# Performance work log

Hardware: AMD Instinct MI355X
Metric: run time of the kernel (lower is better)

Reference implementation:

```python
import jax, jax.numpy as jnp
import numpy as np

S = 3072       # packed sequence length
DIM = 1280     # hidden dim
H = 16         # num heads
HD = DIM // H  # head dim = 80
NEG = -1e9     # additive mask value for cross-segment entries


def setup_inputs() -> dict:
    key = jax.random.key(0)
    ks = jax.random.split(key, 6)
    x = jax.random.normal(ks[0], (S, DIM), jnp.float32)
    # rope angle table [S, HD//2]
    rotary_pos_emb = jax.random.uniform(ks[1], (S, HD // 2), jnp.float32, 0.0, 2.0 * np.pi)
    # 4 equal image segments packed together
    cu_seqlens = jnp.array([0, 768, 1536, 2304, 3072], jnp.int32)
    w_qkv = jax.random.normal(ks[2], (3 * DIM, DIM), jnp.float32) * 0.02
    b_qkv = jax.random.normal(ks[3], (3 * DIM,), jnp.float32) * 0.02
    w_proj = jax.random.normal(ks[4], (DIM, DIM), jnp.float32) * 0.02
    b_proj = jax.random.normal(ks[5], (DIM,), jnp.float32) * 0.02
    return {"x": x, "cu_seqlens": cu_seqlens, "rotary_pos_emb": rotary_pos_emb,
            "w_qkv": w_qkv, "b_qkv": b_qkv, "w_proj": w_proj, "b_proj": b_proj}


def _rope(t, cos, sin):
    # t: [S, H, HD]; cos/sin: [S, 1, HD]
    t1, t2 = jnp.split(t, 2, axis=-1)
    rot = jnp.concatenate([-t2, t1], axis=-1)
    return t * cos + rot * sin


def reference(x, cu_seqlens, rotary_pos_emb, w_qkv, b_qkv, w_proj, b_proj):
    s, d = x.shape
    qkv = (x @ w_qkv.T + b_qkv).reshape(s, 3, H, HD)
    q, k, v = qkv[:, 0], qkv[:, 1], qkv[:, 2]  # each [S, H, HD]

    # NeoX-style rope with tiled (repeated) freqs, computed in fp32
    cos = jnp.cos(rotary_pos_emb)
    sin = jnp.sin(rotary_pos_emb)
    cos = jnp.concatenate([cos, cos], axis=-1)[:, None, :]  # [S,1,HD]
    sin = jnp.concatenate([sin, sin], axis=-1)[:, None, :]
    q = _rope(q.astype(jnp.float32), cos, sin).astype(x.dtype)
    k = _rope(k.astype(jnp.float32), cos, sin).astype(x.dtype)

    # block-diagonal varlen mask from cu_seqlens: segment id per position
    seg = jnp.searchsorted(cu_seqlens, jnp.arange(s), side='right') - 1  # [S]
    mask = jnp.where(seg[:, None] == seg[None, :], 0.0, NEG).astype(x.dtype)  # [S,S]

    scale = 1.0 / np.sqrt(HD).astype(np.float32)
    scores = jnp.einsum('qhd,khd->hqk', q, k) * scale + mask[None]  # [H,S,S]
    attn = jax.nn.softmax(scores, axis=-1)
    out = jnp.einsum('hqk,khd->qhd', attn, v).reshape(s, d)  # [S, DIM]
    return out @ w_proj.T + b_proj
```

## Files before the change

### kernel.cpp

```cpp
#include <hip/hip_runtime.h>


typedef __bf16 bf16;
typedef __bf16 bf16x4 __attribute__((ext_vector_type(4)));
typedef __bf16 bf16x8 __attribute__((ext_vector_type(8)));
typedef float f32x4 __attribute__((ext_vector_type(4)));
typedef float f32x16 __attribute__((ext_vector_type(16)));
typedef unsigned int u32;

constexpr int S = 3072;
constexpr int DIM = 1280;
constexpr int H = 16;
constexpr int HD = 80;
constexpr int KDP = 128;
constexpr int NQKV = 3 * DIM;

constexpr int BM = 192;
constexpr int MB_A = S / BM;
constexpr int NB_B = NQKV / 256;
constexpr int NKT = DIM / 32;
constexpr int ASL = BM * 32 * 2;
constexpr int SLOT = ASL + 16384;

constexpr float QSCALE = 1.4426950408889634f / 8.94427190999916f;

__device__ __forceinline__ void gload_lds16(const void* g, void* l) {
  __builtin_amdgcn_global_load_lds(
      (const __attribute__((address_space(1))) void*)g,
      (__attribute__((address_space(3))) void*)l, 16, 0, 0);
}

__device__ __forceinline__ u32 pkbf2(float a, float b) {
  union { bf16 h[2]; u32 w; } u;
  u.h[0] = (bf16)a; u.h[1] = (bf16)b;
  return u.w;
}

__device__ __forceinline__ int swv(int s) {
  return ((((s >> 3) & 31) ^ ((s & 7) << 2)) << 2);
}

constexpr long PA_CHUNKS = (long)MB_A * NKT * (ASL / 16);
constexpr long PB_CHUNKS = (long)NB_B * NKT * 1024;
constexpr long PW_CHUNKS = (long)DIM * DIM / 8;
constexpr long KP_CHUNKS = (long)H * S * 48 / 8;
constexpr long CS_CHUNKS = (long)S * 40 / 8;
constexpr long TOT_CHUNKS = PA_CHUNKS + PB_CHUNKS + PW_CHUNKS + KP_CHUNKS + CS_CHUNKS;

__global__ __launch_bounds__(256) void pack_inputs(
    const float* __restrict__ x, const float* __restrict__ wq,
    const float* __restrict__ wp, const float* __restrict__ rope,
    bf16* __restrict__ pA, bf16* __restrict__ pB, bf16* __restrict__ wp16,
    bf16* __restrict__ Kb, float* __restrict__ ctab, float* __restrict__ stab) {
  long t = (long)blockIdx.x * 256 + threadIdx.x;
  if (t < PA_CHUNKS) {
    const int blk = (int)(t / (NKT * 768)), rem = (int)(t % (NKT * 768));
    const int kt = rem / 768, c = rem - kt * 768;
    const int lin = c * 16;
    const int logi = lin ^ (((lin >> 7) & 7) << 4);
    const int row = logi >> 6, col = (logi & 63) >> 1;
    const float* src = x + (size_t)(blk * BM + row) * DIM + kt * 32 + col;
    float4 v0 = *(const float4*)src;
    float4 v1 = *(const float4*)(src + 4);
    bf16x8 o = {(bf16)v0.x, (bf16)v0.y, (bf16)v0.z, (bf16)v0.w,
                (bf16)v1.x, (bf16)v1.y, (bf16)v1.z, (bf16)v1.w};
    *(bf16x8*)(pA + t * 8) = o;
  } else if (t < PA_CHUNKS + PB_CHUNKS) {
    long t2 = t - PA_CHUNKS;
    const int blk = (int)(t2 / (NKT * 1024)), rem = (int)(t2 % (NKT * 1024));
    const int kt = rem >> 10, c = rem & 1023;
    const int lin = c * 16;
    const int logi = lin ^ (((lin >> 7) & 7) << 4);
    const int row = logi >> 6, col = (logi & 63) >> 1;
    int grow = blk * 256 + row;
    if (grow < 2560) {
      const int ty = grow / 1280, rm = grow % 1280;
      const int h = rm / 80, p = rm % 80;
      grow = ty * 1280 + h * 80 + (p >> 1) + (p & 1) * 40;
    }
    const float* src = wq + (size_t)grow * DIM + kt * 32 + col;
    float4 v0 = *(const float4*)src;
    float4 v1 = *(const float4*)(src + 4);
    bf16x8 o = {(bf16)v0.x, (bf16)v0.y, (bf16)v0.z, (bf16)v0.w,
                (bf16)v1.x, (bf16)v1.y, (bf16)v1.z, (bf16)v1.w};
    *(bf16x8*)(pB + t2 * 8) = o;
  } else if (t < PA_CHUNKS + PB_CHUNKS + PW_CHUNKS) {
    long t2 = t - PA_CHUNKS - PB_CHUNKS;
    const float* src = wp + t2 * 8;
    float4 v0 = *(const float4*)src;
    float4 v1 = *(const float4*)(src + 4);
    bf16x8 o = {(bf16)v0.x, (bf16)v0.y, (bf16)v0.z, (bf16)v0.w,
                (bf16)v1.x, (bf16)v1.y, (bf16)v1.z, (bf16)v1.w};
    *(bf16x8*)(wp16 + t2 * 8) = o;
  } else if (t < PA_CHUNKS + PB_CHUNKS + PW_CHUNKS + KP_CHUNKS) {
    long t2 = t - PA_CHUNKS - PB_CHUNKS - PW_CHUNKS;
    const int h = (int)(t2 / (S * 6)), r = (int)(t2 % (S * 6));
    const int s = r / 6, cc = r % 6;
    bf16x8 z = {};
    *(bf16x8*)(Kb + ((size_t)h * S + s) * KDP + 80 + cc * 8) = z;
  } else {
    long t3 = t - PA_CHUNKS - PB_CHUNKS - PW_CHUNKS - KP_CHUNKS;
#pragma unroll
    for (int k = 0; k < 8; k++) {
      const int idx = (int)(t3 * 8 + k);
      const int s = idx / 40, a = idx % 40;
      float sn, cs;
      __sincosf(rope[idx], &sn, &cs);
      ctab[a * S + s] = cs;
      stab[a * S + s] = sn;
    }
  }
}

__global__ __launch_bounds__(512, 2) void gemm256(
    const bf16* __restrict__ pA, const bf16* __restrict__ pB,
    const float* __restrict__ bias, const float* __restrict__ ctab,
    const float* __restrict__ stab, bf16* __restrict__ Qb,
    bf16* __restrict__ Kb, bf16* __restrict__ VTb) {
  extern __shared__ char lds[];
  const int tid = threadIdx.x;
  const int w = tid >> 6, lane = tid & 63;
  const int r15 = lane & 15, b4 = lane >> 4;
  const int wr = w >> 2, wc = w & 3;
  const int nwg = gridDim.x * gridDim.y;
  const int orig = blockIdx.y * gridDim.x + blockIdx.x;
  const int xcd = orig % 8, loc = orig / 8;
  const int qq = nwg / 8, rq = nwg % 8;
  const int swzid =
      (xcd < rq ? xcd * (qq + 1) : rq * (qq + 1) + (xcd - rq) * qq) + loc;
  const int nb = swzid % gridDim.x, mb = swzid / gridDim.x;
  const int m0 = mb * BM;
  const char* aPanel = (const char*)pA + (size_t)mb * NKT * ASL;
  const char* bPanel = (const char*)pB + (size_t)nb * NKT * 16384;
  auto stageA = [&](int kt) {
    char* s = lds + (kt & 3) * SLOT;
    const char* g = aPanel + (size_t)kt * ASL;
    gload_lds16(g + tid * 16, s + tid * 16);
    if (tid < 256)
      gload_lds16(g + 8192 + tid * 16, s + 8192 + tid * 16);
  };
  auto stageB = [&](int kt) {
    char* s = lds + (kt & 3) * SLOT + ASL;
    const char* g = bPanel + (size_t)kt * 16384;
    gload_lds16(g + tid * 16, s + tid * 16);
    gload_lds16(g + 8192 + tid * 16, s + 8192 + tid * 16);
  };
  f32x4 acc[6][4] = {};
  stageA(0); stageB(0); stageA(1); stageB(1); stageA(2); stageB(2);
  if (tid < 256) asm volatile("s_waitcnt vmcnt(8)" ::: "memory");
  else           asm volatile("s_waitcnt vmcnt(6)" ::: "memory");
  __builtin_amdgcn_s_barrier();
  for (int kt = 0; kt < NKT; ++kt) {
    const char* As = lds + (kt & 3) * SLOT;
    const char* Bs = As + ASL;
    const bool pf = (kt + 3 < NKT);
    bf16x8 afr[3], bfr[4];
#pragma unroll
    for (int i = 0; i < 3; i++) {
      int a = (wr * 96 + i * 16 + r15) * 64 + b4 * 16;
      a ^= ((a >> 7) & 7) << 4;
      afr[i] = *(const bf16x8*)(As + a);
    }
#pragma unroll
    for (int j = 0; j < 4; j++) {
      int a = (wc * 64 + j * 16 + r15) * 64 + b4 * 16;
      a ^= ((a >> 7) & 7) << 4;
      bfr[j] = *(const bf16x8*)(Bs + a);
    }
    if (pf) stageA(kt + 3);
    asm volatile("" ::: "memory");
    __builtin_amdgcn_s_barrier();
    __builtin_amdgcn_s_setprio(1);
#pragma unroll
    for (int i = 0; i < 3; i++)
#pragma unroll
      for (int j = 0; j < 4; j++)
        acc[i][j] = __builtin_amdgcn_mfma_f32_16x16x32_bf16(afr[i], bfr[j],
                                                            acc[i][j], 0, 0, 0);
    __builtin_amdgcn_s_setprio(0);
    asm volatile("" ::: "memory");
    __builtin_amdgcn_s_barrier();
#pragma unroll
    for (int i = 0; i < 3; i++) {
      int a = (wr * 96 + 48 + i * 16 + r15) * 64 + b4 * 16;
      a ^= ((a >> 7) & 7) << 4;
      afr[i] = *(const bf16x8*)(As + a);
    }
    if (pf) stageB(kt + 3);
    asm volatile("" ::: "memory");
    __builtin_amdgcn_s_barrier();
    __builtin_amdgcn_s_setprio(1);
#pragma unroll
    for (int i = 0; i < 3; i++)
#pragma unroll
      for (int j = 0; j < 4; j++)
        acc[3 + i][j] = __builtin_amdgcn_mfma_f32_16x16x32_bf16(
            afr[i], bfr[j], acc[3 + i][j], 0, 0, 0);
    __builtin_amdgcn_s_setprio(0);
    const int rem = NKT - 2 - kt;
    if (tid < 256) {
      if (rem >= 2)      asm volatile("s_waitcnt vmcnt(8)" ::: "memory");
      else if (rem == 1) asm volatile("s_waitcnt vmcnt(4)" ::: "memory");
      else if (rem == 0) asm volatile("s_waitcnt vmcnt(0)" ::: "memory");
      else               asm volatile("" ::: "memory");
    } else {
      if (rem >= 2)      asm volatile("s_waitcnt vmcnt(6)" ::: "memory");
      else if (rem == 1) asm volatile("s_waitcnt vmcnt(3)" ::: "memory");
      else if (rem == 0) asm volatile("s_waitcnt vmcnt(0)" ::: "memory");
      else               asm volatile("" ::: "memory");
    }
    __builtin_amdgcn_s_barrier();
  }
  const int n0 = nb * 256;
  const int type = n0 / 1280;
  const int cpart0 = n0 - type * 1280;
  if (type < 2) {
#pragma unroll
    for (int j = 0; j < 4; j++) {
      const int c = wc * 64 + j * 16 + r15;
      const int cp = cpart0 + c;
      const int h = cp / 80, p = cp % 80;
      const int d = (p >> 1) + (p & 1) * 40;
      const float bv = bias[type * 1280 + h * 80 + d];
      const int a = p >> 1;
#pragma unroll
      for (int i = 0; i < 6; i++) {
        const int sl = wr * 96 + i * 16 + b4 * 4;
        f32x4 cs4 = *(const f32x4*)&ctab[a * S + m0 + sl];
        f32x4 sn4 = *(const f32x4*)&stab[a * S + m0 + sl];
#pragma unroll
        for (int r = 0; r < 4; r++) {
          float v = acc[i][j][r] + bv;
          float ov = __shfl_xor(v, 1);
          float res = (p & 1) ? (v * cs4[r] + ov * sn4[r])
                              : (v * cs4[r] - ov * sn4[r]);
          if (type == 0) res *= QSCALE;
          *(bf16*)(lds + (sl + r) * 512 + ((2 * c) ^ (((sl + r) & 7) << 4))) =
              (bf16)res;
        }
      }
    }
    __syncthreads();
#pragma unroll
    for (int t = 0; t < 12; t++) {
      const int task = t * 512 + tid;
      const int sl = task >> 5, c = (task & 31) * 8;
      bf16x8 v = *(const bf16x8*)(lds + sl * 512 + ((2 * c) ^ ((sl & 7) << 4)));
      const int cp = cpart0 + c, h = cp / 80, p = cp % 80;
      bf16* dst = type ? Kb + ((size_t)h * S + m0 + sl) * KDP + p
                       : Qb + ((size_t)h * S + m0 + sl) * HD + p;
      *(bf16x8*)dst = v;
    }
  } else {
#pragma unroll
    for (int j = 0; j < 4; j++) {
      const int c = wc * 64 + j * 16 + r15;
      const float bv = bias[2560 + cpart0 + c];
#pragma unroll
      for (int i = 0; i < 6; i++) {
        const int sl = wr * 96 + i * 16 + b4 * 4;
#pragma unroll
        for (int r = 0; r < 4; r++) {
          *(bf16*)(lds + (sl + r) * 512 + ((2 * c) ^ swv(sl + r))) =
              (bf16)(acc[i][j][r] + bv);
        }
      }
    }
    __syncthreads();
#pragma unroll
    for (int t = 0; t < 12; t++) {
      const int task = t * 512 + tid;
      const int c = task & 255, s0 = (task >> 8) * 8;
      union { bf16 h[8]; bf16x8 v; } o;
#pragma unroll
      for (int e = 0; e < 8; e++)
        o.h[e] = *(const bf16*)(lds + (s0 + e) * 512 + ((2 * c) ^ swv(s0 + e)));
      const int cp = cpart0 + c, h = cp / 80, d = cp % 80;
      *(bf16x8*)(VTb + ((size_t)(h * 80 + d)) * S + m0 + s0) = o.v;
    }
  }
}

__global__ __launch_bounds__(256) void gemm_proj(
    const bf16* __restrict__ A, const bf16* __restrict__ B,
    const float* __restrict__ bias, float* __restrict__ Cout, int M, int N,
    int K) {
  __shared__ bf16 Al[2][64 * 32];
  __shared__ bf16 Bl[2][128 * 32];
  const int tid = threadIdx.x;
  const int w = tid >> 6, lane = tid & 63;
  const int r15 = lane & 15, b4 = lane >> 4;
  const int nwg = gridDim.x * gridDim.y;
  const int orig = blockIdx.y * gridDim.x + blockIdx.x;
  const int swzid = (orig & 7) * (nwg >> 3) + (orig >> 3);
  const int bx = swzid % gridDim.x, by = swzid / gridDim.x;
  const int m0 = by * 64, n0 = bx * 128;
  const int wm = (w >> 1) * 32, wn = (w & 1) * 64;
  f32x4 acc[2][4] = {};
  const int row0 = tid >> 2, ko0 = (tid & 3) * 8;
  const bf16* Ar = A + (size_t)(m0 + row0) * K + ko0;
  const bf16* Br0 = B + (size_t)(n0 + row0) * K + ko0;
  const bf16* Br1 = B + (size_t)(n0 + row0 + 64) * K + ko0;

  auto stage = [&](int buf, int k0) {
    gload_lds16(Ar + k0, (char*)Al[buf] + tid * 16);
    gload_lds16(Br0 + k0, (char*)Bl[buf] + tid * 16);
    gload_lds16(Br1 + k0, (char*)Bl[buf] + 4096 + tid * 16);
  };

  stage(0, 0);
  int cur = 0;
  for (int k0 = 0; k0 < K; k0 += 32) {
    __syncthreads();
    if (k0 + 32 < K) stage(cur ^ 1, k0 + 32);
    bf16x8 af[2], bfr[4];
#pragma unroll
    for (int i = 0; i < 2; i++)
      af[i] = *(const bf16x8*)((const char*)Al[cur] + (wm + i * 16 + r15) * 64 + b4 * 16);
#pragma unroll
    for (int j = 0; j < 4; j++)
      bfr[j] = *(const bf16x8*)((const char*)Bl[cur] + (wn + j * 16 + r15) * 64 + b4 * 16);
#pragma unroll
    for (int i = 0; i < 2; i++)
#pragma unroll
      for (int j = 0; j < 4; j++)
        acc[i][j] = __builtin_amdgcn_mfma_f32_16x16x32_bf16(af[i], bfr[j], acc[i][j], 0, 0, 0);
    cur ^= 1;
  }
#pragma unroll
  for (int j = 0; j < 4; j++) {
    const int n = n0 + wn + j * 16 + r15;
    const float bv = bias[n];
#pragma unroll
    for (int i = 0; i < 2; i++) {
      const int mr = m0 + wm + i * 16 + b4 * 4;
#pragma unroll
      for (int r = 0; r < 4; r++)
        Cout[(size_t)(mr + r) * N + n] = acc[i][j][r] + bv;
    }
  }
}

__global__ __launch_bounds__(256, 3) void attn_kern(
    const bf16* __restrict__ Qg, const bf16* __restrict__ Kg,
    const bf16* __restrict__ Vg, const int* __restrict__ cu, int nseg,
    bf16* __restrict__ Out) {
  __shared__ bf16 Kl[2][64 * 128];
  __shared__ bf16 Vl[2][80 * 64];
  const int tid = threadIdx.x, w = tid >> 6, lane = tid & 63;
  const int r31 = lane & 31, hi = lane >> 5;
  const int pair = w >> 1, qs = w & 1;
  const int pt = tid & 127;
  const int nwg = gridDim.x;
  const int orig = blockIdx.x;
  const int swzb = (orig & 7) * (nwg >> 3) + (orig >> 3);
  const int h = swzb / 48, qb = swzb % 48;
  const int q = qb * 64 + qs * 32 + r31;
  int sq = 0, eq = S, lo = 0, hik = S;
  {
    const int qlo = qb * 64, qhi = qb * 64 + 63;
#pragma unroll
    for (int i = 0; i < 8; i++) {
      if (i >= nseg) break;
      int a = cu[i], b = cu[i + 1];
      if (q >= a && q < b) { sq = a; eq = b; }
      if (qlo >= a && qlo < b) lo = a;
      if (qhi >= a && qhi < b) hik = b;
    }
  }
  bf16x8 qf[5];
  {
    const bf16* qrow = Qg + ((size_t)h * S + q) * HD + hi * 8;
#pragma unroll
    for (int kk = 0; kk < 5; kk++) qf[kk] = *(const bf16x8*)(qrow + kk * 16);
  }
  int kdst[8], ksrc[8], vdst[5], vsrc[5];
#pragma unroll
  for (int c = 0; c < 8; c++) {
    int lin = (c * 128 + pt) * 16;
    int row = lin >> 8, colb = (lin & 255) ^ ((row & 15) << 4);
    kdst[c] = lin; ksrc[c] = row * KDP + colb / 2;
  }
#pragma unroll
  for (int c = 0; c < 5; c++) {
    int lin = (c * 128 + pt) * 16;
    int row = lin >> 7, colb = (lin & 127) ^ ((row & 7) << 4);
    vdst[c] = lin; vsrc[c] = row * S + colb / 2;
  }
  const bf16* Kbase = Kg + (size_t)h * S * KDP;
  const bf16* Vbase = Vg + (size_t)h * HD * S;
  char* Klp = (char*)Kl[pair];
  char* Vlp = (char*)Vl[pair];
  auto stage = [&](int k0) {
#pragma unroll
    for (int c = 0; c < 8; c++)
      gload_lds16(Kbase + (size_t)k0 * KDP + ksrc[c], Klp + kdst[c]);
#pragma unroll
    for (int c = 0; c < 5; c++)
      gload_lds16(Vbase + vsrc[c] + k0, Vlp + vdst[c]);
  };
  f32x16 o0 = {}, o1 = {}, o2 = {};
  float m = -1e30f, l = 0.f;
  const int nt = (hik - lo) >> 6;
  const int nit = (nt + 1) >> 1;
  for (int i = 0; i < nit; ++i) {
    const int t = 2 * i + pair;
    const bool act = t < nt;
    const int k0 = lo + t * 64;
    __syncthreads();
    if (act) stage(k0);
    asm volatile("s_waitcnt vmcnt(0)" ::: "memory");
    __syncthreads();
    if (!act) continue;
    f32x16 st0 = {}, st1 = {};
    __builtin_amdgcn_s_setprio(1);
#pragma unroll
    for (int kk = 0; kk < 5; kk++) {
      const int colb = kk * 32 + hi * 16;
      bf16x8 kf0 = *(const bf16x8*)(Klp + r31 * 256 + (colb ^ ((r31 & 15) << 4)));
      bf16x8 kf1 = *(const bf16x8*)(Klp + (32 + r31) * 256 + (colb ^ ((r31 & 15) << 4)));
      st0 = __builtin_amdgcn_mfma_f32_32x32x16_bf16(kf0, qf[kk], st0, 0, 0, 0);
      st1 = __builtin_amdgcn_mfma_f32_32x32x16_bf16(kf1, qf[kk], st1, 0, 0, 0);
    }
    __builtin_amdgcn_s_setprio(0);
    float tm = -3e38f;
    if (k0 >= sq && k0 + 63 < eq) {
#pragma unroll
      for (int j = 0; j < 16; j++) {
        tm = fmaxf(tm, st0[j]);
        tm = fmaxf(tm, st1[j]);
      }
    } else {
#pragma unroll
      for (int j = 0; j < 16; j++) {
        const int crow = (j & 3) + 8 * (j >> 2) + 4 * hi;
        int key0 = k0 + crow, key1 = k0 + 32 + crow;
        st0[j] = (key0 >= sq && key0 < eq) ? st0[j] : -1e30f;
        st1[j] = (key1 >= sq && key1 < eq) ? st1[j] : -1e30f;
        tm = fmaxf(tm, st0[j]);
        tm = fmaxf(tm, st1[j]);
      }
    }
    tm = fmaxf(tm, __shfl_xor(tm, 32));
    if (!__all(tm <= m + 8.f)) {
      const float mn = fmaxf(m, tm);
      const float alpha = __builtin_amdgcn_exp2f(m - mn);
      o0 *= alpha; o1 *= alpha; o2 *= alpha;
      l *= alpha;
      m = mn;
    }
    float rs = 0.f;
    u32 wd0[4][2], wd1[4][2];
#pragma unroll
    for (int g2 = 0; g2 < 4; g2++) {
#pragma unroll
      for (int hh = 0; hh < 2; hh++) {
        float a0 = __builtin_amdgcn_exp2f(st0[g2 * 4 + 2 * hh] - m);
        float a1 = __builtin_amdgcn_exp2f(st0[g2 * 4 + 2 * hh + 1] - m);
        float b0 = __builtin_amdgcn_exp2f(st1[g2 * 4 + 2 * hh] - m);
        float b1 = __builtin_amdgcn_exp2f(st1[g2 * 4 + 2 * hh + 1] - m);
        rs += a0 + a1 + b0 + b1;
        wd0[g2][hh] = pkbf2(a0, a1);
        wd1[g2][hh] = pkbf2(b0, b1);
      }
    }
    rs += __shfl_xor(rs, 32);
    l += rs;
    __builtin_amdgcn_s_setprio(1);
#pragma unroll
    for (int kk = 0; kk < 4; kk++) {
      const int g2o = (kk & 1) * 2 + hi;
      const int g2s = (kk & 1) * 2 + (hi ^ 1);
      u32 own0, own1, snd0, snd1;
      if (kk < 2) {
        own0 = wd0[g2o][0]; own1 = wd0[g2o][1];
        snd0 = wd0[g2s][0]; snd1 = wd0[g2s][1];
      } else {
        own0 = wd1[g2o][0]; own1 = wd1[g2o][1];
        snd0 = wd1[g2s][0]; snd1 = wd1[g2s][1];
      }
      u32 rc0 = (u32)__shfl_xor((int)snd0, 32);
      u32 rc1 = (u32)__shfl_xor((int)snd1, 32);
      union { u32 w[4]; bf16x8 v; } pf;
      if (hi == 0) { pf.w[0] = own0; pf.w[1] = own1; pf.w[2] = rc0; pf.w[3] = rc1; }
      else         { pf.w[0] = rc0;  pf.w[1] = rc1;  pf.w[2] = own0; pf.w[3] = own1; }
      const int colb = kk * 32 + hi * 16;
#pragma unroll
      for (int mt = 0; mt < 3; mt++) {
        int row = mt * 32 + r31;
        row = row < HD ? row : 0;
        bf16x8 vf = *(const bf16x8*)(Vlp + row * 128 + (colb ^ ((row & 7) << 4)));
        f32x16* op = mt == 0 ? &o0 : (mt == 1 ? &o1 : &o2);
        *op = __builtin_amdgcn_mfma_f32_32x32x16_bf16(vf, pf.v, *op, 0, 0, 0);
      }
    }
    __builtin_amdgcn_s_setprio(0);
  }
  __syncthreads();
  float* mb = (float*)Kl;
  if (pair == 1) {
    float* d = mb + ((size_t)qs * 64 + lane) * 50;
    d[0] = m; d[1] = l;
#pragma unroll
    for (int j = 0; j < 16; j++) { d[2 + j] = o0[j]; d[18 + j] = o1[j]; d[34 + j] = o2[j]; }
  }
  __syncthreads();
  if (pair == 0) {
    const float* d = mb + ((size_t)qs * 64 + lane) * 50;
    const float pm = d[0], pl = d[1];
    const float mn = fmaxf(m, pm);
    const float a = __builtin_amdgcn_exp2f(m - mn);
    const float b = __builtin_amdgcn_exp2f(pm - mn);
    const float lt = l * a + pl * b;
    const float inv = 1.f / lt;
    bf16* orow = Out + (size_t)q * DIM + h * HD;
#pragma unroll
    for (int rg = 0; rg < 4; rg++) {
      bf16x4 v0, v1;
#pragma unroll
      for (int e = 0; e < 4; e++) {
        v0[e] = (bf16)((o0[rg * 4 + e] * a + d[2 + rg * 4 + e] * b) * inv);
        v1[e] = (bf16)((o1[rg * 4 + e] * a + d[18 + rg * 4 + e] * b) * inv);
      }
      *(bf16x4*)(orow + 8 * rg + 4 * hi) = v0;
      *(bf16x4*)(orow + 32 + 8 * rg + 4 * hi) = v1;
    }
#pragma unroll
    for (int rg = 0; rg < 2; rg++) {
      bf16x4 v2;
#pragma unroll
      for (int e = 0; e < 4; e++)
        v2[e] = (bf16)((o2[rg * 4 + e] * a + d[34 + rg * 4 + e] * b) * inv);
      *(bf16x4*)(orow + 64 + 8 * rg + 4 * hi) = v2;
    }
  }
}

extern "C" void kernel_launch(void* const* d_in, const int* in_sizes, int n_in,
                              void* d_out, int out_size, void* d_ws,
                              size_t ws_size, hipStream_t stream) {
  const float* x = (const float*)d_in[0];
  const int* cu = (const int*)d_in[1];
  const float* rope = (const float*)d_in[2];
  const float* w_qkv = (const float*)d_in[3];
  const float* b_qkv = (const float*)d_in[4];
  const float* w_proj = (const float*)d_in[5];
  const float* b_proj = (const float*)d_in[6];
  const int nseg = in_sizes[1] - 1;

  bf16* pA = (bf16*)d_ws;
  bf16* pB = pA + (size_t)S * DIM;
  bf16* wp16 = pB + (size_t)NQKV * DIM;
  bf16* Qb = wp16 + (size_t)DIM * DIM;
  bf16* Kb = Qb + (size_t)H * S * HD;
  bf16* VTb = Kb + (size_t)H * S * KDP;
  float* ctab = (float*)(VTb + (size_t)H * HD * S);
  float* stab = ctab + (size_t)S * 40;
  bf16* attn16 = pA;

  pack_inputs<<<(int)(TOT_CHUNKS / 256), 256, 0, stream>>>(
      x, w_qkv, w_proj, rope, pA, pB, wp16, Kb, ctab, stab);
  gemm256<<<dim3(NB_B, MB_A), 512, 114688, stream>>>(
      pA, pB, b_qkv, ctab, stab, Qb, Kb, VTb);
  attn_kern<<<H * 48, 256, 0, stream>>>(Qb, Kb, VTb, cu, nseg, attn16);
  gemm_proj<<<dim3(DIM / 128, S / 64), 256, 0, stream>>>(
      attn16, wp16, b_proj, (float*)d_out, S, DIM, DIM);
}
```

Before: 111.4 us.

## Split attention keys across waves with pre-tiled K/V and no block syncs

New measurement: 118.2 us. 6.2% more time.

```diff
diff --git a/kernel.cpp b/kernel.cpp
--- a/kernel.cpp
+++ b/kernel.cpp
@@ -12,8 +12,8 @@
 constexpr int DIM = 1280;
 constexpr int H = 16;
 constexpr int HD = 80;
-constexpr int KDP = 128;
 constexpr int NQKV = 3 * DIM;
+constexpr int NT32 = S / 32;
 
 constexpr int BM = 192;
 constexpr int MB_A = S / BM;
@@ -21,6 +21,9 @@
 constexpr int NKT = DIM / 32;
 constexpr int ASL = BM * 32 * 2;
 constexpr int SLOT = ASL + 16384;
+
+constexpr int KIMG = 32 * 256;
+constexpr int VIMG = 40 * 128;
 
 constexpr float QSCALE = 1.4426950408889634f / 8.94427190999916f;
 
@@ -94,10 +97,13 @@
     *(bf16x8*)(wp16 + t2 * 8) = o;
   } else if (t < PA_CHUNKS + PB_CHUNKS + PW_CHUNKS + KP_CHUNKS) {
     long t2 = t - PA_CHUNKS - PB_CHUNKS - PW_CHUNKS;
-    const int h = (int)(t2 / (S * 6)), r = (int)(t2 % (S * 6));
-    const int s = r / 6, cc = r % 6;
+    const int h = (int)(t2 / (S * 6)), r0 = (int)(t2 % (S * 6));
+    const int s = r0 / 6, cc = r0 % 6;
+    const int tile = s >> 5, r = s & 31;
+    const int p = 80 + cc * 8;
     bf16x8 z = {};
-    *(bf16x8*)(Kb + ((size_t)h * S + s) * KDP + 80 + cc * 8) = z;
+    *(bf16x8*)((char*)Kb + (size_t)(h * NT32 + tile) * KIMG + r * 256 +
+               ((2 * p) ^ ((r & 15) << 4))) = z;
   } else {
     long t3 = t - PA_CHUNKS - PB_CHUNKS - PW_CHUNKS - KP_CHUNKS;
 #pragma unroll
@@ -247,9 +253,13 @@
       const int sl = task >> 5, c = (task & 31) * 8;
       bf16x8 v = *(const bf16x8*)(lds + sl * 512 + ((2 * c) ^ ((sl & 7) << 4)));
       const int cp = cpart0 + c, h = cp / 80, p = cp % 80;
-      bf16* dst = type ? Kb + ((size_t)h * S + m0 + sl) * KDP + p
-                       : Qb + ((size_t)h * S + m0 + sl) * HD + p;
-      *(bf16x8*)dst = v;
+      if (type == 0) {
+        *(bf16x8*)(Qb + ((size_t)h * S + m0 + sl) * HD + p) = v;
+      } else {
+        const int s = m0 + sl, tile = s >> 5, r = s & 31;
+        *(bf16x8*)((char*)Kb + (size_t)(h * NT32 + tile) * KIMG + r * 256 +
+                   ((2 * p) ^ ((r & 15) << 4))) = v;
+      }
     }
   } else {
 #pragma unroll
@@ -276,7 +286,10 @@
       for (int e = 0; e < 8; e++)
         o.h[e] = *(const bf16*)(lds + (s0 + e) * 512 + ((2 * c) ^ swv(s0 + e)));
       const int cp = cpart0 + c, h = cp / 80, d = cp % 80;
-      *(bf16x8*)(VTb + ((size_t)(h * 80 + d)) * S + m0 + s0) = o.v;
+      const int s0g = m0 + s0, tile = s0g >> 5, sin = s0g & 31;
+      const int jrow = d >> 1;
+      *(bf16x8*)((char*)VTb + (size_t)(h * NT32 + tile) * VIMG + jrow * 128 +
+                 (((d & 1) * 64 + sin * 2) ^ ((jrow & 7) << 4))) = o.v;
     }
   }
 }
@@ -342,30 +355,25 @@
 }
 
 __global__ __launch_bounds__(256, 3) void attn_kern(
-    const bf16* __restrict__ Qg, const bf16* __restrict__ Kg,
-    const bf16* __restrict__ Vg, const int* __restrict__ cu, int nseg,
+    const bf16* __restrict__ Qg, const bf16* __restrict__ Kt,
+    const bf16* __restrict__ Vt, const int* __restrict__ cu, int nseg,
     bf16* __restrict__ Out) {
-  __shared__ bf16 Kl[2][64 * 128];
-  __shared__ bf16 Vl[2][80 * 64];
+  __shared__ char SL[4][KIMG + VIMG];
   const int tid = threadIdx.x, w = tid >> 6, lane = tid & 63;
   const int r31 = lane & 31, hi = lane >> 5;
-  const int pair = w >> 1, qs = w & 1;
-  const int pt = tid & 127;
   const int nwg = gridDim.x;
   const int orig = blockIdx.x;
   const int swzb = (orig & 7) * (nwg >> 3) + (orig >> 3);
-  const int h = swzb / 48, qb = swzb % 48;
-  const int q = qb * 64 + qs * 32 + r31;
-  int sq = 0, eq = S, lo = 0, hik = S;
+  const int h = swzb / 96, qb = swzb % 96;
+  const int q = qb * 32 + r31;
+  int lo = 0, hik = S;
   {
-    const int qlo = qb * 64, qhi = qb * 64 + 63;
+    const int qlo = qb * 32;
 #pragma unroll
     for (int i = 0; i < 8; i++) {
       if (i >= nseg) break;
       int a = cu[i], b = cu[i + 1];
-      if (q >= a && q < b) { sq = a; eq = b; }
-      if (qlo >= a && qlo < b) lo = a;
-      if (qhi >= a && qhi < b) hik = b;
+      if (qlo >= a && qlo < b) { lo = a; hik = b; }
     }
   }
   bf16x8 qf[5];
@@ -374,73 +382,34 @@
 #pragma unroll
     for (int kk = 0; kk < 5; kk++) qf[kk] = *(const bf16x8*)(qrow + kk * 16);
   }
-  int kdst[8], ksrc[8], vdst[5], vsrc[5];
-#pragma unroll
-  for (int c = 0; c < 8; c++) {
-    int lin = (c * 128 + pt) * 16;
-    int row = lin >> 8, colb = (lin & 255) ^ ((row & 15) << 4);
-    kdst[c] = lin; ksrc[c] = row * KDP + colb / 2;
-  }
-#pragma unroll
-  for (int c = 0; c < 5; c++) {
-    int lin = (c * 128 + pt) * 16;
-    int row = lin >> 7, colb = (lin & 127) ^ ((row & 7) << 4);
-    vdst[c] = lin; vsrc[c] = row * S + colb / 2;
-  }
-  const bf16* Kbase = Kg + (size_t)h * S * KDP;
-  const bf16* Vbase = Vg + (size_t)h * HD * S;
-  char* Klp = (char*)Kl[pair];
-  char* Vlp = (char*)Vl[pair];
-  auto stage = [&](int k0) {
-#pragma unroll
-    for (int c = 0; c < 8; c++)
-      gload_lds16(Kbase + (size_t)k0 * KDP + ksrc[c], Klp + kdst[c]);
-#pragma unroll
-    for (int c = 0; c < 5; c++)
-      gload_lds16(Vbase + vsrc[c] + k0, Vlp + vdst[c]);
-  };
+  char* myK = SL[w];
+  char* myV = SL[w] + KIMG;
+  const char* Kh = (const char*)Kt + (size_t)h * NT32 * KIMG;
+  const char* Vh = (const char*)Vt + (size_t)h * NT32 * VIMG;
   f32x16 o0 = {}, o1 = {}, o2 = {};
   float m = -1e30f, l = 0.f;
-  const int nt = (hik - lo) >> 6;
-  const int nit = (nt + 1) >> 1;
-  for (int i = 0; i < nit; ++i) {
-    const int t = 2 * i + pair;
-    const bool act = t < nt;
-    const int k0 = lo + t * 64;
-    __syncthreads();
-    if (act) stage(k0);
+  const int nt = (hik - lo) >> 5;
+  const int t0 = lo >> 5;
+  for (int t = w; t < nt; t += 4) {
+    const char* gK = Kh + (size_t)(t0 + t) * KIMG;
+    const char* gV = Vh + (size_t)(t0 + t) * VIMG;
+#pragma unroll
+    for (int c = 0; c < 8; c++)
+      gload_lds16(gK + (c * 64 + lane) * 16, myK + (c * 64 + lane) * 16);
+#pragma unroll
+    for (int c = 0; c < 5; c++)
+      gload_lds16(gV + (c * 64 + lane) * 16, myV + (c * 64 + lane) * 16);
     asm volatile("s_waitcnt vmcnt(0)" ::: "memory");
-    __syncthreads();
-    if (!act) continue;
-    f32x16 st0 = {}, st1 = {};
-    __builtin_amdgcn_s_setprio(1);
+    f32x16 st0 = {};
 #pragma unroll
     for (int kk = 0; kk < 5; kk++) {
-      const int colb = kk * 32 + hi * 16;
-      bf16x8 kf0 = *(const bf16x8*)(Klp + r31 * 256 + (colb ^ ((r31 & 15) << 4)));
-      bf16x8 kf1 = *(const bf16x8*)(Klp + (32 + r31) * 256 + (colb ^ ((r31 & 15) << 4)));
-      st0 = __builtin_amdgcn_mfma_f32_32x32x16_bf16(kf0, qf[kk], st0, 0, 0, 0);
-      st1 = __builtin_amdgcn_mfma_f32_32x32x16_bf16(kf1, qf[kk], st1, 0, 0, 0);
-    }
-    __builtin_amdgcn_s_setprio(0);
+      bf16x8 kf = *(const bf16x8*)(myK + r31 * 256 +
+                                   ((kk * 32 + hi * 16) ^ ((r31 & 15) << 4)));
+      st0 = __builtin_amdgcn_mfma_f32_32x32x16_bf16(kf, qf[kk], st0, 0, 0, 0);
+    }
     float tm = -3e38f;
-    if (k0 >= sq && k0 + 63 < eq) {
-#pragma unroll
-      for (int j = 0; j < 16; j++) {
-        tm = fmaxf(tm, st0[j]);
-        tm = fmaxf(tm, st1[j]);
-      }
-    } else {
-#pragma unroll
-      for (int j = 0; j < 16; j++) {
-        const int crow = (j & 3) + 8 * (j >> 2) + 4 * hi;
-        int key0 = k0 + crow, key1 = k0 + 32 + crow;
-        st0[j] = (key0 >= sq && key0 < eq) ? st0[j] : -1e30f;
-        st1[j] = (key1 >= sq && key1 < eq) ? st1[j] : -1e30f;
-        tm = fmaxf(tm, st0[j]);
-        tm = fmaxf(tm, st1[j]);
-      }
-    }
+#pragma unroll
+    for (int j = 0; j < 16; j++) tm = fmaxf(tm, st0[j]);
     tm = fmaxf(tm, __shfl_xor(tm, 32));
     if (!__all(tm <= m + 8.f)) {
       const float mn = fmaxf(m, tm);
@@ -450,87 +419,84 @@
       m = mn;
     }
     float rs = 0.f;
-    u32 wd0[4][2], wd1[4][2];
+    u32 wd0[4][2];
 #pragma unroll
     for (int g2 = 0; g2 < 4; g2++) {
 #pragma unroll
       for (int hh = 0; hh < 2; hh++) {
         float a0 = __builtin_amdgcn_exp2f(st0[g2 * 4 + 2 * hh] - m);
         float a1 = __builtin_amdgcn_exp2f(st0[g2 * 4 + 2 * hh + 1] - m);
-        float b0 = __builtin_amdgcn_exp2f(st1[g2 * 4 + 2 * hh] - m);
-        float b1 = __builtin_amdgcn_exp2f(st1[g2 * 4 + 2 * hh + 1] - m);
-        rs += a0 + a1 + b0 + b1;
+        rs += a0 + a1;
         wd0[g2][hh] = pkbf2(a0, a1);
-        wd1[g2][hh] = pkbf2(b0, b1);
       }
     }
     rs += __shfl_xor(rs, 32);
     l += rs;
-    __builtin_amdgcn_s_setprio(1);
-#pragma unroll
-    for (int kk = 0; kk < 4; kk++) {
-      const int g2o = (kk & 1) * 2 + hi;
-      const int g2s = (kk & 1) * 2 + (hi ^ 1);
-      u32 own0, own1, snd0, snd1;
-      if (kk < 2) {
-        own0 = wd0[g2o][0]; own1 = wd0[g2o][1];
-        snd0 = wd0[g2s][0]; snd1 = wd0[g2s][1];
-      } else {
-        own0 = wd1[g2o][0]; own1 = wd1[g2o][1];
-        snd0 = wd1[g2s][0]; snd1 = wd1[g2s][1];
-      }
+#pragma unroll
+    for (int kk = 0; kk < 2; kk++) {
+      const int g2o = kk * 2 + hi;
+      const int g2s = kk * 2 + (hi ^ 1);
+      u32 own0 = wd0[g2o][0], own1 = wd0[g2o][1];
+      u32 snd0 = wd0[g2s][0], snd1 = wd0[g2s][1];
       u32 rc0 = (u32)__shfl_xor((int)snd0, 32);
       u32 rc1 = (u32)__shfl_xor((int)snd1, 32);
       union { u32 w[4]; bf16x8 v; } pf;
       if (hi == 0) { pf.w[0] = own0; pf.w[1] = own1; pf.w[2] = rc0; pf.w[3] = rc1; }
       else         { pf.w[0] = rc0;  pf.w[1] = rc1;  pf.w[2] = own0; pf.w[3] = own1; }
-      const int colb = kk * 32 + hi * 16;
 #pragma unroll
       for (int mt = 0; mt < 3; mt++) {
-        int row = mt * 32 + r31;
-        row = row < HD ? row : 0;
-        bf16x8 vf = *(const bf16x8*)(Vlp + row * 128 + (colb ^ ((row & 7) << 4)));
+        int d = mt * 32 + r31;
+        d = d < HD ? d : 0;
+        const int jrow = d >> 1;
+        bf16x8 vf = *(const bf16x8*)(myV + jrow * 128 +
+                                     (((d & 1) * 64 + kk * 32 + hi * 16) ^
+                                      ((jrow & 7) << 4)));
         f32x16* op = mt == 0 ? &o0 : (mt == 1 ? &o1 : &o2);
         *op = __builtin_amdgcn_mfma_f32_32x32x16_bf16(vf, pf.v, *op, 0, 0, 0);
       }
     }
-    __builtin_amdgcn_s_setprio(0);
   }
   __syncthreads();
-  float* mb = (float*)Kl;
-  if (pair == 1) {
-    float* d = mb + ((size_t)qs * 64 + lane) * 50;
+  float* mb = (float*)SL;
+  if (w) {
+    float* d = mb + ((size_t)(w - 1) * 64 + lane) * 50;
     d[0] = m; d[1] = l;
 #pragma unroll
     for (int j = 0; j < 16; j++) { d[2 + j] = o0[j]; d[18 + j] = o1[j]; d[34 + j] = o2[j]; }
   }
   __syncthreads();
-  if (pair == 0) {
-    const float* d = mb + ((size_t)qs * 64 + lane) * 50;
-    const float pm = d[0], pl = d[1];
-    const float mn = fmaxf(m, pm);
-    const float a = __builtin_amdgcn_exp2f(m - mn);
-    const float b = __builtin_amdgcn_exp2f(pm - mn);
-    const float lt = l * a + pl * b;
-    const float inv = 1.f / lt;
+  if (w == 0) {
+#pragma unroll
+    for (int s = 0; s < 3; s++) {
+      const float* d = mb + ((size_t)s * 64 + lane) * 50;
+      const float pm = d[0], pl = d[1];
+      const float mn = fmaxf(m, pm);
+      const float a = __builtin_amdgcn_exp2f(m - mn);
+      const float b = __builtin_amdgcn_exp2f(pm - mn);
+#pragma unroll
+      for (int j = 0; j < 16; j++) {
+        o0[j] = o0[j] * a + d[2 + j] * b;
+        o1[j] = o1[j] * a + d[18 + j] * b;
+        o2[j] = o2[j] * a + d[34 + j] * b;
+      }
+      l = l * a + pl * b;
+      m = mn;
+    }
+    const float inv = 1.f / l;
     bf16* orow = Out + (size_t)q * DIM + h * HD;
 #pragma unroll
     for (int rg = 0; rg < 4; rg++) {
-      bf16x4 v0, v1;
-#pragma unroll
-      for (int e = 0; e < 4; e++) {
-        v0[e] = (bf16)((o0[rg * 4 + e] * a + d[2 + rg * 4 + e] * b) * inv);
-        v1[e] = (bf16)((o1[rg * 4 + e] * a + d[18 + rg * 4 + e] * b) * inv);
-      }
+      bf16x4 v0 = {(bf16)(o0[rg * 4] * inv), (bf16)(o0[rg * 4 + 1] * inv),
+                   (bf16)(o0[rg * 4 + 2] * inv), (bf16)(o0[rg * 4 + 3] * inv)};
       *(bf16x4*)(orow + 8 * rg + 4 * hi) = v0;
+      bf16x4 v1 = {(bf16)(o1[rg * 4] * inv), (bf16)(o1[rg * 4 + 1] * inv),
+                   (bf16)(o1[rg * 4 + 2] * inv), (bf16)(o1[rg * 4 + 3] * inv)};
       *(bf16x4*)(orow + 32 + 8 * rg + 4 * hi) = v1;
     }
 #pragma unroll
     for (int rg = 0; rg < 2; rg++) {
-      bf16x4 v2;
-#pragma unroll
-      for (int e = 0; e < 4; e++)
-        v2[e] = (bf16)((o2[rg * 4 + e] * a + d[34 + rg * 4 + e] * b) * inv);
+      bf16x4 v2 = {(bf16)(o2[rg * 4] * inv), (bf16)(o2[rg * 4 + 1] * inv),
+                   (bf16)(o2[rg * 4 + 2] * inv), (bf16)(o2[rg * 4 + 3] * inv)};
       *(bf16x4*)(orow + 64 + 8 * rg + 4 * hi) = v2;
     }
   }
@@ -553,7 +519,7 @@
   bf16* wp16 = pB + (size_t)NQKV * DIM;
   bf16* Qb = wp16 + (size_t)DIM * DIM;
   bf16* Kb = Qb + (size_t)H * S * HD;
-  bf16* VTb = Kb + (size_t)H * S * KDP;
+  bf16* VTb = Kb + (size_t)H * S * 128;
   float* ctab = (float*)(VTb + (size_t)H * HD * S);
   float* stab = ctab + (size_t)S * 40;
   bf16* attn16 = pA;
@@ -562,7 +528,7 @@
       x, w_qkv, w_proj, rope, pA, pB, wp16, Kb, ctab, stab);
   gemm256<<<dim3(NB_B, MB_A), 512, 114688, stream>>>(
       pA, pB, b_qkv, ctab, stab, Qb, Kb, VTb);
-  attn_kern<<<H * 48, 256, 0, stream>>>(Qb, Kb, VTb, cu, nseg, attn16);
+  attn_kern<<<H * 96, 256, 0, stream>>>(Qb, Kb, VTb, cu, nseg, attn16);
   gemm_proj<<<dim3(DIM / 128, S / 64), 256, 0, stream>>>(
       attn16, wp16, b_proj, (float*)d_out, S, DIM, DIM);
 }
```
